# Performance work log

Hardware: AMD Instinct MI355X
Metric: run time of the kernel (lower is better)

Reference implementation:

```python
import jax, jax.numpy as jnp
import numpy as np

NUM_HEADS = 16


def _rope_tables(seq_len, head_dim, dtype):
    # angles[n, j] = n * 10000^(-2j/head_dim)
    pos = jnp.arange(seq_len, dtype=jnp.float32)
    inv = jnp.power(10000.0, -2.0 * jnp.arange(head_dim // 2, dtype=jnp.float32) / head_dim)
    ang = pos[:, None] * inv[None, :]                     # [N, D/2]
    # repeat_interleave(.., 2): [c0,c0,c1,c1,...]
    cos = jnp.repeat(jnp.cos(ang), 2, axis=-1).astype(dtype)  # [N, D]
    sin = jnp.repeat(jnp.sin(ang), 2, axis=-1).astype(dtype)  # [N, D]
    return cos[None, None], sin[None, None]               # [1,1,N,D]


def _rotate_half_interleaved(x):
    # stack([-x[...,1::2], x[...,::2]], -1).reshape_as(x)
    x2 = jnp.stack([-x[..., 1::2], x[..., ::2]], axis=-1)
    return x2.reshape(x.shape)


def setup_inputs() -> dict:
    key = jax.random.key(0)
    k0, k1, k2, k3 = jax.random.split(key, 4)
    B, N, C = 2, 2048, 1024
    s = 1.0 / np.sqrt(C)
    return {
        "x": jax.random.normal(k0, (B, N, C), dtype=jnp.float32),
        "Wq": jax.random.normal(k1, (C, C), dtype=jnp.float32) * s,
        "Wk": jax.random.normal(k2, (C, C), dtype=jnp.float32) * s,
        "Wv": jax.random.normal(k3, (C, C), dtype=jnp.float32) * s,
    }


def reference(x, Wq, Wk, Wv):
    B, N, C = x.shape
    H = NUM_HEADS
    D = C // H
    scale = D ** -0.5

    def heads(y):  # [B,N,C] -> [B,H,N,D]
        return y.reshape(B, N, H, D).transpose(0, 2, 1, 3)

    # nn.Linear: y = x @ W.T
    q = heads(x @ Wq.T)
    k = heads(x @ Wk.T)
    v = heads(x @ Wv.T)

    cos, sin = _rope_tables(N, D, x.dtype)
    q = q * cos + _rotate_half_interleaved(q) * sin
    k = k * cos + _rotate_half_interleaved(k) * sin

    attn = jnp.einsum("bhnd,bhmd->bhnm", q, k) * scale
    attn = jax.nn.softmax(attn, axis=-1)          # dropout p=0.0 -> identity
    out = jnp.einsum("bhnm,bhmd->bhnd", attn, v)
    return out.transpose(0, 2, 1, 3).reshape(B, N, C)
```

## Files before the change

### kernel.cpp

```cpp
#include <hip/hip_runtime.h>

typedef _Float16 f16;
typedef _Float16 f16x2 __attribute__((ext_vector_type(2)));
typedef _Float16 f16x8 __attribute__((ext_vector_type(8)));
typedef _Float16 f16x4 __attribute__((ext_vector_type(4)));
typedef float f32x4 __attribute__((ext_vector_type(4)));

#define GAS(p) ((const __attribute__((address_space(1))) void*)(p))
#define LAS(p) ((__attribute__((address_space(3))) void*)(p))

__device__ __forceinline__ f32x4 mfma16(f16x8 a, f16x8 b, f32x4 c) {
  return __builtin_amdgcn_mfma_f32_16x16x32_f16(a, b, c, 0, 0, 0);
}

__device__ __forceinline__ f16x2 cvt2(float a, float b) {
  return __builtin_bit_cast(f16x2, __builtin_amdgcn_cvt_pkrtz(a, b));
}

__device__ __forceinline__ float fexp2(float x) {
#if __has_builtin(__builtin_amdgcn_exp2f)
  return __builtin_amdgcn_exp2f(x);
#else
  float r;
  asm("v_exp_f32 %0, %1" : "=v"(r) : "v"(x));
  return r;
#endif
}

__device__ __forceinline__ void stage_tile(const f16* __restrict__ grow0,
                                           int stride_f16, f16* lds, int t) {
  int r = t >> 3;
  int sw = ((t & 7) ^ (r & 7)) * 8;
  __builtin_amdgcn_global_load_lds(GAS(grow0 + r * stride_f16 + sw),
                                   LAS(lds + t * 8), 16, 0, 0);
}

__global__ void convall(const float* __restrict__ x, const float* __restrict__ wq,
                        const float* __restrict__ wk, const float* __restrict__ wv,
                        f16* __restrict__ xh, f16* __restrict__ wh,
                        float* __restrict__ cosT, float* __restrict__ sinT) {
  int bid = blockIdx.x;
  if (bid >= 3584) {
    int idx = (bid - 3584) * 256 + threadIdx.x;
    int n = idx >> 5, jj = idx & 31;
    float inv = powf(10000.0f, -(float)jj * (1.0f / 32.0f));
    float ang = (float)n * inv;
    cosT[idx] = cosf(ang);
    sinT[idx] = sinf(ang);
    return;
  }
  const float* s;
  f16* d;
  int boff;
  if (bid < 2048)      { s = x;  d = xh;            boff = bid; }
  else if (bid < 2560) { s = wq; d = wh;            boff = bid - 2048; }
  else if (bid < 3072) { s = wk; d = wh + 1048576;  boff = bid - 2560; }
  else                 { s = wv; d = wh + 2097152;  boff = bid - 3072; }
  int i = (boff * 256 + threadIdx.x) * 8;
  float4 a = *(const float4*)(s + i);
  float4 b = *(const float4*)(s + i + 4);
  f16x8 o = {(f16)a.x, (f16)a.y, (f16)a.z, (f16)a.w,
             (f16)b.x, (f16)b.y, (f16)b.z, (f16)b.w};
  *(f16x8*)(d + i) = o;
}

__global__ __launch_bounds__(256, 3) void qkv_gemm(
    const f16* __restrict__ X, const f16* __restrict__ W,
    const float* __restrict__ cosT, const float* __restrict__ sinT,
    f16* __restrict__ Q, f16* __restrict__ K, f16* __restrict__ Vt) {
  __shared__ f16 As[128 * 64];
  __shared__ f16 Bs[128 * 64];
  const int tid = threadIdx.x;
  const int wv = tid >> 6, lane = tid & 63;
  const int lin = blockIdx.x;
  const int xcd = lin & 7, idx = lin >> 3;
  const int m0 = (xcd * 4 + (idx & 3)) * 128;
  const int n0 = (idx >> 2) * 128;
  const int cl = lane & 15, g = lane >> 4;
  const int wr = (wv >> 1) * 64, wc = (wv & 1) * 64;
  const int vx = cl & 7;

  f32x4 acc[4][4] = {};
  const f16* ga = X + (size_t)m0 * 1024;
  const f16* gb = W + (size_t)n0 * 1024;

  for (int kt = 0; kt < 1024; kt += 64) {
    __syncthreads();
#pragma unroll
    for (int rd = 0; rd < 4; ++rd) {
      stage_tile(ga + kt, 1024, As, tid + rd * 256);
      stage_tile(gb + kt, 1024, Bs, tid + rd * 256);
    }
    __syncthreads();
#pragma unroll
    for (int kk = 0; kk < 2; ++kk) {
      f16x8 a[4], bf[4];
#pragma unroll
      for (int mi = 0; mi < 4; ++mi)
        a[mi] = *(const f16x8*)(As + (wr + mi * 16 + cl) * 64 +
                                (((kk * 4 + g) ^ vx) << 3));
#pragma unroll
      for (int ni = 0; ni < 4; ++ni)
        bf[ni] = *(const f16x8*)(Bs + (wc + ni * 16 + cl) * 64 +
                                 (((kk * 4 + g) ^ vx) << 3));
#pragma unroll
      for (int mi = 0; mi < 4; ++mi)
#pragma unroll
        for (int ni = 0; ni < 4; ++ni)
          acc[mi][ni] = mfma16(a[mi], bf[ni], acc[mi][ni]);
    }
  }

  const int p = n0 >> 10;
  for (int mi = 0; mi < 4; ++mi) {
    int rbase = m0 + wr + mi * 16 + g * 4;
    for (int ni = 0; ni < 4; ++ni) {
      int gc = n0 + wc + ni * 16 + cl;
      int f = gc & 1023;
      int h = f >> 6, d = f & 63;
      if (p < 2) {
        int j = d >> 1;
        f16* dst = (p == 0) ? Q : K;
        float sc = (p == 0) ? 0.18033688011f : 1.0f;
        for (int r = 0; r < 4; ++r) {
          int row = rbase + r;
          int bb = row >> 11, n = row & 2047;
          float co = cosT[n * 32 + j], si = sinT[n * 32 + j];
          float v = acc[mi][ni][r];
          float pr = __shfl_xor(v, 1);
          float o = (d & 1) ? (v * co + pr * si) : (v * co - pr * si);
          dst[((bb * 16 + h) * 2048 + n) * 64 + d] = (f16)(o * sc);
        }
      } else {
        int bb = rbase >> 11, n = rbase & 2047;
        int np = (n & ~31) | (((n >> 2) & 3) << 3) | (((n >> 4) & 1) << 2);
        f16x4 pk = {(f16)acc[mi][ni][0], (f16)acc[mi][ni][1],
                    (f16)acc[mi][ni][2], (f16)acc[mi][ni][3]};
        *(f16x4*)(Vt + (size_t)((bb * 16 + h) * 64 + d) * 2048 + np) = pk;
      }
    }
  }
}

__global__ __launch_bounds__(256, 2) void attn(
    const f16* __restrict__ Q, const f16* __restrict__ K,
    const f16* __restrict__ Vt, float* __restrict__ out) {
  __shared__ f16 Ks[2][2][4096];
  __shared__ f16 Vs[2][2][4096];
  const int tid = threadIdx.x;
  const int w = tid >> 6, lane = tid & 63;
  const int cl = lane & 15, g = lane >> 4;
  const int id = blockIdx.x;
  const int xcd = id & 7, j = id >> 3;
  const int bh = xcd * 4 + (j >> 4);
  const int b = bh >> 4, h = bh & 15;
  const int qb = (j & 15) * 128 + w * 32;
  const f16* Qp = Q + (size_t)bh * (2048 * 64);
  const f16* Kp = K + (size_t)bh * (2048 * 64);
  const f16* Vp = Vt + (size_t)bh * (64 * 2048);

  f16x8 bq[2][2];
#pragma unroll
  for (int qh = 0; qh < 2; ++qh) {
    bq[qh][0] = *(const f16x8*)(Qp + (qb + qh * 16 + cl) * 64 + g * 8);
    bq[qh][1] = *(const f16x8*)(Qp + (qb + qh * 16 + cl) * 64 + 32 + g * 8);
  }

  f32x4 acc[2][4] = {};
  f32x4 acc1[2] = {};
  const f16x8 kones = {(f16)1, (f16)1, (f16)1, (f16)1,
                       (f16)1, (f16)1, (f16)1, (f16)1};
  const int vx = cl & 7;
  const f32x4 z4 = {0.f, 0.f, 0.f, 0.f};
  union PB { f16x8 v; f16x2 hx[4]; };
  struct AS { f32x4 s[2][4]; f16x8 vf[2][4]; };

  auto STAGE = [&](int it, int bf) {
    const f16* kp = Kp + (size_t)it * 8192;
    const f16* vp = Vp + (size_t)it * 128;
#pragma unroll
    for (int hh = 0; hh < 2; ++hh) {
      stage_tile(kp + hh * 4096, 64, Ks[bf][hh], tid);
      stage_tile(kp + hh * 4096, 64, Ks[bf][hh], tid + 256);
      stage_tile(vp + hh * 64, 2048, Vs[bf][hh], tid);
      stage_tile(vp + hh * 64, 2048, Vs[bf][hh], tid + 256);
    }
  };

  auto APH = [&](const f16* kb, const f16* vb, AS& S) {
    f16x8 a0[4], a1[4];
#pragma unroll
    for (int i = 0; i < 4; ++i) {
      const f16* kr = kb + (i * 16 + cl) * 64;
      a0[i] = *(const f16x8*)(kr + ((g ^ vx) << 3));
      a1[i] = *(const f16x8*)(kr + (((4 + g) ^ vx) << 3));
    }
#pragma unroll
    for (int ks = 0; ks < 2; ++ks)
#pragma unroll
      for (int d = 0; d < 4; ++d)
        S.vf[ks][d] = *(const f16x8*)(vb + (d * 16 + cl) * 64 +
                                      (((ks * 4 + g) ^ vx) << 3));
    __builtin_amdgcn_s_setprio(1);
#pragma unroll
    for (int qh = 0; qh < 2; ++qh)
#pragma unroll
      for (int i = 0; i < 4; ++i)
        S.s[qh][i] = mfma16(a1[i], bq[qh][1], mfma16(a0[i], bq[qh][0], z4));
    __builtin_amdgcn_s_setprio(0);
  };

  auto BPH = [&](AS& S) {
    PB pb[2][2];
#pragma unroll
    for (int qh = 0; qh < 2; ++qh) {
      float p0 = fexp2(S.s[qh][0][0]), p1 = fexp2(S.s[qh][0][1]);
      float p2 = fexp2(S.s[qh][0][2]), p3 = fexp2(S.s[qh][0][3]);
      float p4 = fexp2(S.s[qh][1][0]), p5 = fexp2(S.s[qh][1][1]);
      float p6 = fexp2(S.s[qh][1][2]), p7 = fexp2(S.s[qh][1][3]);
      float p8 = fexp2(S.s[qh][2][0]), p9 = fexp2(S.s[qh][2][1]);
      float pa = fexp2(S.s[qh][2][2]), pc = fexp2(S.s[qh][2][3]);
      float pd = fexp2(S.s[qh][3][0]), pe = fexp2(S.s[qh][3][1]);
      float pf = fexp2(S.s[qh][3][2]), pg = fexp2(S.s[qh][3][3]);
      pb[qh][0].hx[0] = cvt2(p0, p1); pb[qh][0].hx[1] = cvt2(p2, p3);
      pb[qh][0].hx[2] = cvt2(p4, p5); pb[qh][0].hx[3] = cvt2(p6, p7);
      pb[qh][1].hx[0] = cvt2(p8, p9); pb[qh][1].hx[1] = cvt2(pa, pc);
      pb[qh][1].hx[2] = cvt2(pd, pe); pb[qh][1].hx[3] = cvt2(pf, pg);
    }
    __builtin_amdgcn_s_setprio(1);
#pragma unroll
    for (int ks = 0; ks < 2; ++ks) {
#pragma unroll
      for (int d = 0; d < 4; ++d) {
        acc[0][d] = mfma16(S.vf[ks][d], pb[0][ks].v, acc[0][d]);
        acc[1][d] = mfma16(S.vf[ks][d], pb[1][ks].v, acc[1][d]);
      }
      acc1[0] = mfma16(kones, pb[0][ks].v, acc1[0]);
      acc1[1] = mfma16(kones, pb[1][ks].v, acc1[1]);
    }
    __builtin_amdgcn_s_setprio(0);
  };

  STAGE(0, 0);
  asm volatile("s_waitcnt vmcnt(0)" ::: "memory");
  __builtin_amdgcn_s_barrier();
  STAGE(1, 1);
  AS P, Qs;
  APH(Ks[0][0], Vs[0][0], P);

  for (int it = 0; it < 16; ++it) {
    const int c = it & 1;
    APH(Ks[c][1], Vs[c][1], Qs);
    BPH(P);
    if (it < 15) {
      asm volatile("s_waitcnt vmcnt(0)" ::: "memory");
      __builtin_amdgcn_s_barrier();
      if (it + 2 < 16) STAGE(it + 2, c);
      APH(Ks[c ^ 1][0], Vs[c ^ 1][0], P);
      BPH(Qs);
    } else {
      BPH(Qs);
    }
  }

#pragma unroll
  for (int qh = 0; qh < 2; ++qh) {
    float inv = 1.0f / acc1[qh][0];
    float* ob = out + (size_t)(b * 2048 + qb + qh * 16 + cl) * 1024 +
                h * 64 + g * 4;
#pragma unroll
    for (int d = 0; d < 4; ++d) {
      float4 o = {acc[qh][d][0] * inv, acc[qh][d][1] * inv,
                  acc[qh][d][2] * inv, acc[qh][d][3] * inv};
      *(float4*)(ob + (size_t)d * 16) = o;
    }
  }
}

extern "C" void kernel_launch(void* const* d_in, const int* in_sizes, int n_in,
                              void* d_out, int out_size, void* d_ws, size_t ws_size,
                              hipStream_t stream) {
  const float* x  = (const float*)d_in[0];
  const float* Wq = (const float*)d_in[1];
  const float* Wk = (const float*)d_in[2];
  const float* Wv = (const float*)d_in[3];
  float* out = (float*)d_out;
  char* ws = (char*)d_ws;

  f16* xh   = (f16*)(ws);
  f16* wh   = (f16*)(ws + 8388608);
  f16* Qr   = (f16*)(ws + 14680064);
  f16* Kr   = (f16*)(ws + 23068672);
  f16* Vt   = (f16*)(ws + 31457280);
  float* cosT = (float*)(ws + 39845888);
  float* sinT = (float*)(ws + 40108032);

  convall<<<3840, 256, 0, stream>>>(x, Wq, Wk, Wv, xh, wh, cosT, sinT);

  qkv_gemm<<<768, 256, 0, stream>>>(xh, wh, cosT, sinT, Qr, Kr, Vt);

  attn<<<512, 256, 0, stream>>>(Qr, Kr, Vt, out);
}
```

Baseline: 81.48 us.

## Halve attention block to two waves with 64-key tiles and more blocks

The attention kernel now runs 128-thread blocks, each covering 64 query rows instead of 128, and launches twice as many blocks. Each pipeline stage loads a single 64-key tile into a two-slot LDS ring, so each block needs half the shared memory. The main loop is restructured to wait and barrier once per half-tile. The aim is more resident blocks and better latency hiding. In exchange, each K/V tile is reused by fewer queries, which doubles total K/V traffic, and the loop synchronises more often.

```diff
diff --git a/kernel.cpp b/kernel.cpp
--- a/kernel.cpp
+++ b/kernel.cpp
@@ -142,19 +142,19 @@
   }
 }
 
-__global__ __launch_bounds__(256, 2) void attn(
+__global__ __launch_bounds__(128, 2) void attn(
     const f16* __restrict__ Q, const f16* __restrict__ K,
     const f16* __restrict__ Vt, float* __restrict__ out) {
-  __shared__ f16 Ks[2][2][4096];
-  __shared__ f16 Vs[2][2][4096];
+  __shared__ f16 Ks[2][4096];
+  __shared__ f16 Vs[2][4096];
   const int tid = threadIdx.x;
   const int w = tid >> 6, lane = tid & 63;
   const int cl = lane & 15, g = lane >> 4;
   const int id = blockIdx.x;
   const int xcd = id & 7, j = id >> 3;
-  const int bh = xcd * 4 + (j >> 4);
+  const int bh = xcd * 4 + (j >> 5);
   const int b = bh >> 4, h = bh & 15;
-  const int qb = (j & 15) * 128 + w * 32;
+  const int qb = (j & 31) * 64 + w * 32;
   const f16* Qp = Q + (size_t)bh * (2048 * 64);
   const f16* Kp = K + (size_t)bh * (2048 * 64);
   const f16* Vp = Vt + (size_t)bh * (64 * 2048);
@@ -176,15 +176,12 @@
   struct AS { f32x4 s[2][4]; f16x8 vf[2][4]; };
 
   auto STAGE = [&](int it, int bf) {
-    const f16* kp = Kp + (size_t)it * 8192;
-    const f16* vp = Vp + (size_t)it * 128;
-#pragma unroll
-    for (int hh = 0; hh < 2; ++hh) {
-      stage_tile(kp + hh * 4096, 64, Ks[bf][hh], tid);
-      stage_tile(kp + hh * 4096, 64, Ks[bf][hh], tid + 256);
-      stage_tile(vp + hh * 64, 2048, Vs[bf][hh], tid);
-      stage_tile(vp + hh * 64, 2048, Vs[bf][hh], tid + 256);
-    }
+    const f16* kp = Kp + (size_t)it * 4096;
+    const f16* vp = Vp + (size_t)it * 64;
+#pragma unroll
+    for (int c = 0; c < 4; ++c) stage_tile(kp, 64, Ks[bf], tid + c * 128);
+#pragma unroll
+    for (int c = 0; c < 4; ++c) stage_tile(vp, 2048, Vs[bf], tid + c * 128);
   };
 
   auto APH = [&](const f16* kb, const f16* vb, AS& S) {
@@ -241,27 +238,30 @@
     __builtin_amdgcn_s_setprio(0);
   };
 
+  AS P, Qs;
   STAGE(0, 0);
   asm volatile("s_waitcnt vmcnt(0)" ::: "memory");
   __builtin_amdgcn_s_barrier();
   STAGE(1, 1);
-  AS P, Qs;
-  APH(Ks[0][0], Vs[0][0], P);
-
-  for (int it = 0; it < 16; ++it) {
-    const int c = it & 1;
-    APH(Ks[c][1], Vs[c][1], Qs);
+  APH(Ks[0], Vs[0], P);
+
+  for (int t = 0; t < 15; ++t) {
+    asm volatile("s_waitcnt vmcnt(0)" ::: "memory");
+    __builtin_amdgcn_s_barrier();
+    STAGE(2 * t + 2, 0);
+    APH(Ks[1], Vs[1], Qs);
     BPH(P);
-    if (it < 15) {
-      asm volatile("s_waitcnt vmcnt(0)" ::: "memory");
-      __builtin_amdgcn_s_barrier();
-      if (it + 2 < 16) STAGE(it + 2, c);
-      APH(Ks[c ^ 1][0], Vs[c ^ 1][0], P);
-      BPH(Qs);
-    } else {
-      BPH(Qs);
-    }
-  }
+    asm volatile("s_waitcnt vmcnt(0)" ::: "memory");
+    __builtin_amdgcn_s_barrier();
+    if (2 * t + 3 < 32) STAGE(2 * t + 3, 1);
+    APH(Ks[0], Vs[0], P);
+    BPH(Qs);
+  }
+  asm volatile("s_waitcnt vmcnt(0)" ::: "memory");
+  __builtin_amdgcn_s_barrier();
+  APH(Ks[1], Vs[1], Qs);
+  BPH(P);
+  BPH(Qs);
 
 #pragma unroll
   for (int qh = 0; qh < 2; ++qh) {
@@ -299,5 +299,5 @@
 
   qkv_gemm<<<768, 256, 0, stream>>>(xh, wh, cosT, sinT, Qr, Kr, Vt);
 
-  attn<<<512, 256, 0, stream>>>(Qr, Kr, Vt, out);
-}
+  attn<<<1024, 128, 0, stream>>>(Qr, Kr, Vt, out);
+}
```

After: 85.37 us. +4.8%, slower.
